# Kernel optimization log

Hardware: AMD Instinct MI355X
Metric: run time of the kernel (lower is better)

Reference implementation:

```python
import jax, jax.numpy as jnp
import numpy as np

INPUT_DIM = 2048
N_EXPERTS = 64
K = 2


def setup_inputs() -> dict:
    key = jax.random.key(0)
    kx, kw, kb = jax.random.split(key, 3)
    x = jax.random.normal(kx, (4, 4096, INPUT_DIM), dtype=jnp.float32)
    # nn.Linear(input_dim, n_experts): weight [n_experts, input_dim], bias [n_experts]
    bound = 1.0 / np.sqrt(INPUT_DIM)
    W = jax.random.uniform(kw, (N_EXPERTS, INPUT_DIM), minval=-bound, maxval=bound, dtype=jnp.float32)
    b = jax.random.uniform(kb, (N_EXPERTS,), minval=-bound, maxval=bound, dtype=jnp.float32)
    return {"x": x, "W": W, "b": b}


def reference(x, W, b):
    # logits: [B, S, E]
    logits = jnp.einsum('bsd,ed->bse', x, W) + b
    topk_vals, topk_indices = jax.lax.top_k(logits, K)  # over last (expert) axis
    gate_probs = jax.nn.softmax(topk_vals, axis=-1)
    return gate_probs, topk_indices
```

## Files before the change

### kernel.cpp

```cpp
#include <hip/hip_runtime.h>
#include <math.h>
#include <stdint.h>

typedef _Float16 half8 __attribute__((ext_vector_type(8)));
typedef float floatx4 __attribute__((ext_vector_type(4)));

#define NTOK 16384
#define DIM  2048
#define NEXP 64
#define TPB  32
#define NBLK (NTOK / TPB)
#define KSPL 4
#define KW   (DIM / KSPL)
#define NST  (KW / 32)
#define RSTR 68
#define REDF (KSPL * TPB * RSTR)

__device__ __forceinline__ void split8(const float4& v0, const float4& v1,
                                       half8& hi, half8& lo) {
    const float av[8] = {v0.x, v0.y, v0.z, v0.w, v1.x, v1.y, v1.z, v1.w};
#pragma unroll
    for (int j = 0; j < 8; j++) {
        const _Float16 hh = (_Float16)av[j];
        hi[j] = hh;
        lo[j] = (_Float16)((av[j] - (float)hh) * 2048.0f);
    }
}

__global__ __launch_bounds__(256, 2)
void gating_kernel(const float* __restrict__ x, const float* __restrict__ W,
                   const float* __restrict__ bias, float* __restrict__ out)
{
    __shared__ float red[REDF];
    __shared__ float bsh[NEXP];

    const int tid  = threadIdx.x;
    const int lane = tid & 63;
    const int ks   = tid >> 6;
    const int col  = lane & 15;
    const int quad = lane >> 4;
    const int tok0 = blockIdx.x * TPB;
    const int k0   = ks * KW;

    if (tid < NEXP) bsh[tid] = bias[tid];

    const float* pA[2];
#pragma unroll
    for (int m = 0; m < 2; m++)
        pA[m] = x + (size_t)(tok0 + m * 16 + col) * DIM + k0 + quad * 8;
    const float* pB[4];
#pragma unroll
    for (int t = 0; t < 4; t++)
        pB[t] = W + (size_t)(t * 16 + col) * DIM + k0 + quad * 8;

    float4 Ab[3][2][2];
    float4 Bb[2][4][2];
    floatx4 accm[2][4];
    floatx4 accl[2][4];
#pragma unroll
    for (int m = 0; m < 2; m++)
#pragma unroll
        for (int t = 0; t < 4; t++) { accm[m][t] = (floatx4){0,0,0,0}; accl[m][t] = (floatx4){0,0,0,0}; }

#pragma unroll
    for (int s = 0; s < 2; s++)
#pragma unroll
        for (int m = 0; m < 2; m++)
#pragma unroll
            for (int h = 0; h < 2; h++)
                Ab[s][m][h] = *(const float4*)(pA[m] + s * 32 + h * 4);
#pragma unroll
    for (int t = 0; t < 4; t++)
#pragma unroll
        for (int h = 0; h < 2; h++)
            Bb[0][t][h] = *(const float4*)(pB[t] + h * 4);

#pragma unroll
    for (int s = 0; s < NST; s++) {
        if (s + 2 < NST) {
#pragma unroll
            for (int m = 0; m < 2; m++)
#pragma unroll
                for (int h = 0; h < 2; h++)
                    Ab[(s + 2) % 3][m][h] = *(const float4*)(pA[m] + (s + 2) * 32 + h * 4);
        }
        if (s + 1 < NST) {
#pragma unroll
            for (int t = 0; t < 4; t++)
#pragma unroll
                for (int h = 0; h < 2; h++)
                    Bb[(s + 1) & 1][t][h] = *(const float4*)(pB[t] + (s + 1) * 32 + h * 4);
        }
        half8 ah[2], al[2];
#pragma unroll
        for (int m = 0; m < 2; m++)
            split8(Ab[s % 3][m][0], Ab[s % 3][m][1], ah[m], al[m]);
#pragma unroll
        for (int t = 0; t < 4; t++) {
            half8 bh, bl;
            split8(Bb[s & 1][t][0], Bb[s & 1][t][1], bh, bl);
#pragma unroll
            for (int m = 0; m < 2; m++) {
                accm[m][t] = __builtin_amdgcn_mfma_f32_16x16x32_f16(ah[m], bh, accm[m][t], 0, 0, 0);
                accl[m][t] = __builtin_amdgcn_mfma_f32_16x16x32_f16(ah[m], bl, accl[m][t], 0, 0, 0);
                accl[m][t] = __builtin_amdgcn_mfma_f32_16x16x32_f16(al[m], bh, accl[m][t], 0, 0, 0);
            }
        }
    }

    const float inv = 1.0f / 2048.0f;
#pragma unroll
    for (int t = 0; t < 4; t++)
#pragma unroll
        for (int m = 0; m < 2; m++)
#pragma unroll
            for (int r = 0; r < 4; r++)
                red[(ks * TPB + m * 16 + quad * 4 + r) * RSTR + t * 16 + col] =
                    accm[m][t][r] + accl[m][t][r] * inv;
    __syncthreads();

    if (tid < TPB) {
        const int tk = tid;
        float v0 = -INFINITY, v1 = -INFINITY;
        int   i0 = 0, i1 = 0;
        for (int e = 0; e < NEXP; e++) {
            const float v = red[(0 * TPB + tk) * RSTR + e]
                          + red[(1 * TPB + tk) * RSTR + e]
                          + red[(2 * TPB + tk) * RSTR + e]
                          + red[(3 * TPB + tk) * RSTR + e] + bsh[e];
            if (v > v0)      { v1 = v0; i1 = i0; v0 = v; i0 = e; }
            else if (v > v1) { v1 = v; i1 = e; }
        }
        const float e1 = expf(v1 - v0);
        const float sden = 1.f + e1;
        const int   g  = tok0 + tk;
        out[2 * g + 0] = 1.f / sden;
        out[2 * g + 1] = e1 / sden;
        out[2 * NTOK + 2 * g + 0] = (float)i0;
        out[2 * NTOK + 2 * g + 1] = (float)i1;
    }
}

extern "C" void kernel_launch(void* const* d_in, const int* in_sizes, int n_in,
                              void* d_out, int out_size, void* d_ws, size_t ws_size,
                              hipStream_t stream) {
    (void)d_ws; (void)ws_size;
    const float* x    = (const float*)d_in[0];
    const float* W    = (const float*)d_in[1];
    const float* bias = (const float*)d_in[2];
    float*       out  = (float*)d_out;
    hipLaunchKernelGGL(gating_kernel, dim3(NBLK), dim3(256), 0, stream,
                       x, W, bias, out);
}
```

Baseline: 226.1 us.

## Split token halves across extra waves to raise occupancy and cut registers

Doubles the block to 512 threads so each wave handles one 16-token half instead of both, which halves the A buffers and accumulators per wave. The B (W) double-buffer prefetch is dropped in favour of loading B right before use within each step. The aim is lower register pressure and more resident waves to hide global memory latency. The cost is that W fragments are now loaded by twice as many waves, and the B loads lose their one-step-ahead prefetch.

Result: slower. 247.6 us (+9.5%).

```diff
diff --git a/kernel.cpp b/kernel.cpp
--- a/kernel.cpp
+++ b/kernel.cpp
@@ -27,7 +27,7 @@
     }
 }
 
-__global__ __launch_bounds__(256, 2)
+__global__ __launch_bounds__(512, 4)
 void gating_kernel(const float* __restrict__ x, const float* __restrict__ W,
                    const float* __restrict__ bias, float* __restrict__ out)
 {
@@ -36,7 +36,9 @@
 
     const int tid  = threadIdx.x;
     const int lane = tid & 63;
-    const int ks   = tid >> 6;
+    const int wid  = tid >> 6;
+    const int ks   = wid & 3;
+    const int mh   = wid >> 2;
     const int col  = lane & 15;
     const int quad = lane >> 4;
     const int tok0 = blockIdx.x * TPB;
@@ -44,67 +46,46 @@
 
     if (tid < NEXP) bsh[tid] = bias[tid];
 
-    const float* pA[2];
-#pragma unroll
-    for (int m = 0; m < 2; m++)
-        pA[m] = x + (size_t)(tok0 + m * 16 + col) * DIM + k0 + quad * 8;
+    const float* pA = x + (size_t)(tok0 + mh * 16 + col) * DIM + k0 + quad * 8;
     const float* pB[4];
 #pragma unroll
     for (int t = 0; t < 4; t++)
         pB[t] = W + (size_t)(t * 16 + col) * DIM + k0 + quad * 8;
 
-    float4 Ab[3][2][2];
-    float4 Bb[2][4][2];
-    floatx4 accm[2][4];
-    floatx4 accl[2][4];
+    float4 Ab[3][2];
+    floatx4 accm[4], accl[4];
 #pragma unroll
-    for (int m = 0; m < 2; m++)
-#pragma unroll
-        for (int t = 0; t < 4; t++) { accm[m][t] = (floatx4){0,0,0,0}; accl[m][t] = (floatx4){0,0,0,0}; }
+    for (int t = 0; t < 4; t++) { accm[t] = (floatx4){0,0,0,0}; accl[t] = (floatx4){0,0,0,0}; }
 
 #pragma unroll
     for (int s = 0; s < 2; s++)
 #pragma unroll
-        for (int m = 0; m < 2; m++)
-#pragma unroll
-            for (int h = 0; h < 2; h++)
-                Ab[s][m][h] = *(const float4*)(pA[m] + s * 32 + h * 4);
-#pragma unroll
-    for (int t = 0; t < 4; t++)
-#pragma unroll
         for (int h = 0; h < 2; h++)
-            Bb[0][t][h] = *(const float4*)(pB[t] + h * 4);
+            Ab[s][h] = *(const float4*)(pA + s * 32 + h * 4);
 
 #pragma unroll
     for (int s = 0; s < NST; s++) {
         if (s + 2 < NST) {
 #pragma unroll
-            for (int m = 0; m < 2; m++)
+            for (int h = 0; h < 2; h++)
+                Ab[(s + 2) % 3][h] = *(const float4*)(pA + (s + 2) * 32 + h * 4);
+        }
+        float4 Bb[4][2];
 #pragma unroll
-                for (int h = 0; h < 2; h++)
-                    Ab[(s + 2) % 3][m][h] = *(const float4*)(pA[m] + (s + 2) * 32 + h * 4);
-        }
-        if (s + 1 < NST) {
+        for (int t = 0; t < 4; t++)
 #pragma unroll
-            for (int t = 0; t < 4; t++)
-#pragma unroll
-                for (int h = 0; h < 2; h++)
-                    Bb[(s + 1) & 1][t][h] = *(const float4*)(pB[t] + (s + 1) * 32 + h * 4);
-        }
-        half8 ah[2], al[2];
-#pragma unroll
-        for (int m = 0; m < 2; m++)
-            split8(Ab[s % 3][m][0], Ab[s % 3][m][1], ah[m], al[m]);
+            for (int h = 0; h < 2; h++)
+                Bb[t][h] = *(const float4*)(pB[t] + s * 32 + h * 4);
+
+        half8 ah, al;
+        split8(Ab[s % 3][0], Ab[s % 3][1], ah, al);
 #pragma unroll
         for (int t = 0; t < 4; t++) {
             half8 bh, bl;
-            split8(Bb[s & 1][t][0], Bb[s & 1][t][1], bh, bl);
-#pragma unroll
-            for (int m = 0; m < 2; m++) {
-                accm[m][t] = __builtin_amdgcn_mfma_f32_16x16x32_f16(ah[m], bh, accm[m][t], 0, 0, 0);
-                accl[m][t] = __builtin_amdgcn_mfma_f32_16x16x32_f16(ah[m], bl, accl[m][t], 0, 0, 0);
-                accl[m][t] = __builtin_amdgcn_mfma_f32_16x16x32_f16(al[m], bh, accl[m][t], 0, 0, 0);
-            }
+            split8(Bb[t][0], Bb[t][1], bh, bl);
+            accm[t] = __builtin_amdgcn_mfma_f32_16x16x32_f16(ah, bh, accm[t], 0, 0, 0);
+            accl[t] = __builtin_amdgcn_mfma_f32_16x16x32_f16(ah, bl, accl[t], 0, 0, 0);
+            accl[t] = __builtin_amdgcn_mfma_f32_16x16x32_f16(al, bh, accl[t], 0, 0, 0);
         }
     }
 
@@ -112,11 +93,9 @@
 #pragma unroll
     for (int t = 0; t < 4; t++)
 #pragma unroll
-        for (int m = 0; m < 2; m++)
-#pragma unroll
-            for (int r = 0; r < 4; r++)
-                red[(ks * TPB + m * 16 + quad * 4 + r) * RSTR + t * 16 + col] =
-                    accm[m][t][r] + accl[m][t][r] * inv;
+        for (int r = 0; r < 4; r++)
+            red[(ks * TPB + mh * 16 + quad * 4 + r) * RSTR + t * 16 + col] =
+                accm[t][r] + accl[t][r] * inv;
     __syncthreads();
 
     if (tid < TPB) {
@@ -149,6 +128,6 @@
     const float* W    = (const float*)d_in[1];
     const float* bias = (const float*)d_in[2];
     float*       out  = (float*)d_out;
-    hipLaunchKernelGGL(gating_kernel, dim3(NBLK), dim3(256), 0, stream,
+    hipLaunchKernelGGL(gating_kernel, dim3(NBLK), dim3(512), 0, stream,
                        x, W, bias, out);
 }
```
